# Optimization experiments

Hardware: AMD Instinct MI355X
Metric: run time of the kernel (lower is better)

## Reference

```python
import jax, jax.numpy as jnp
import numpy as np

N, C, D, H, W = 4, 9, 16, 1024, 1024  # batch, grid channels, grid size, image HxW


def setup_inputs() -> dict:
    key = jax.random.key(0)
    k1, k2, k3, k4 = jax.random.split(key, 4)
    bilateral_grid = jax.random.normal(k1, (N, C, D, D, D), dtype=jnp.float32)
    guidemap = jax.random.uniform(k2, (N, 3, H, W), dtype=jnp.float32)
    conv_w = jax.random.normal(k3, (3, C + 3), dtype=jnp.float32) * 0.1  # 1x1 conv kernel
    conv_b = jax.random.normal(k4, (3,), dtype=jnp.float32) * 0.1
    return {"bilateral_grid": bilateral_grid, "guidemap": guidemap,
            "conv_w": conv_w, "conv_b": conv_b}


def _trilinear_slice(grid, guide):
    # grid: [N, C, D, D, D]; guide: [N, 3, H, W] with values in [0,1]
    n, c, d = grid.shape[0], grid.shape[1], grid.shape[2]
    h, w = guide.shape[2], guide.shape[3]
    grid_flat = grid.reshape(n, c, d * d * d)
    coords = jnp.clip(guide, 0.0, 1.0) * (d - 1)          # [N,3,H,W]
    i0 = jnp.clip(jnp.floor(coords), 0, d - 2).astype(jnp.int32)
    f = coords - i0.astype(coords.dtype)                   # fractional part
    r0, g0, b0 = i0[:, 0], i0[:, 1], i0[:, 2]              # [N,H,W]
    fr, fg, fb = f[:, 0], f[:, 1], f[:, 2]                 # [N,H,W]

    def gather(ir, ig, ib):
        flat = ((ir * d + ig) * d + ib).reshape(n, 1, h * w)
        return jnp.take_along_axis(grid_flat, flat, axis=2)  # [N,C,H*W]

    out = jnp.zeros((n, c, h * w), dtype=grid.dtype)
    for dr in (0, 1):
        for dg in (0, 1):
            for db in (0, 1):
                wgt = ((fr if dr else 1.0 - fr) *
                       (fg if dg else 1.0 - fg) *
                       (fb if db else 1.0 - fb)).reshape(n, 1, h * w)
                out = out + gather(r0 + dr, g0 + dg, b0 + db) * wgt
    return out.reshape(n, c, h, w)


def reference(bilateral_grid, guidemap, conv_w, conv_b):
    res = _trilinear_slice(bilateral_grid, guidemap)       # [N,9,H,W]
    res = jnp.concatenate([res, guidemap], axis=1)         # [N,12,H,W]
    out = jnp.einsum('oi,nihw->nohw', conv_w, res) + conv_b[None, :, None, None]
    return out
```

## Files before the change

kernel.cpp:

```cpp
#include <hip/hip_runtime.h>
#include <hip/hip_bf16.h>

static constexpr int N_ = 4;
static constexpr int C_ = 9;
static constexpr int D_ = 16;
static constexpr int HWp = 1024 * 1024;
static constexpr int CELLS = D_ * D_ * D_;
static constexpr int PT = HWp / 4;
static constexpr int TPB = 512;
static constexpr int BPI = 256;

__device__ __forceinline__ void unpack3(uint2 w, float& x, float& y, float& z) {
    x = __uint_as_float(w.x << 16);
    y = __uint_as_float(w.x & 0xFFFF0000u);
    z = __uint_as_float(w.y << 16);
}

__device__ __forceinline__ float lerp1(float a, float b, float t) {
    return fmaf(b - a, t, a);
}

__global__ __launch_bounds__(TPB) void slice_kernel(
    const float* __restrict__ grid, const float* __restrict__ guide,
    const float* __restrict__ cw, const float* __restrict__ cbias,
    float* __restrict__ out)
{
    __shared__ uint2 sPre[CELLS];

    const int n  = blockIdx.x >> 8;
    const int bi = blockIdx.x & (BPI - 1);

    {
        const float* g = grid + (size_t)n * C_ * CELLS;
#pragma unroll
        for (int k = 0; k < CELLS / TPB; ++k) {
            int cell = k * TPB + threadIdx.x;
            float a0 = 0.f, a1 = 0.f, a2 = 0.f;
#pragma unroll
            for (int c = 0; c < C_; ++c) {
                float v = g[(size_t)c * CELLS + cell];
                a0 = fmaf(cw[c], v, a0);
                a1 = fmaf(cw[12 + c], v, a1);
                a2 = fmaf(cw[24 + c], v, a2);
            }
            unsigned short b0 = __bfloat16_as_ushort(__float2bfloat16(a0));
            unsigned short b1 = __bfloat16_as_ushort(__float2bfloat16(a1));
            unsigned short b2 = __bfloat16_as_ushort(__float2bfloat16(a2));
            uint2 v;
            v.x = (unsigned)b0 | ((unsigned)b1 << 16);
            v.y = (unsigned)b2;
            sPre[cell] = v;
        }
    }
    __syncthreads();

    const float4* gR = (const float4*)(guide + (size_t)(n * 3 + 0) * HWp);
    const float4* gG = (const float4*)(guide + (size_t)(n * 3 + 1) * HWp);
    const float4* gB = (const float4*)(guide + (size_t)(n * 3 + 2) * HWp);
    float4* oR = (float4*)(out + (size_t)(n * 3 + 0) * HWp);
    float4* oG = (float4*)(out + (size_t)(n * 3 + 1) * HWp);
    float4* oB = (float4*)(out + (size_t)(n * 3 + 2) * HWp);

    const float w0r = cw[9],  w0g = cw[10], w0b = cw[11];
    const float w1r = cw[21], w1g = cw[22], w1b = cw[23];
    const float w2r = cw[33], w2g = cw[34], w2b = cw[35];
    const float bi0 = cbias[0], bi1 = cbias[1], bi2 = cbias[2];

    const int base0 = bi * (PT / BPI);

#pragma unroll
    for (int it = 0; it < (PT / BPI) / TPB; ++it) {
        const int p4 = base0 + it * TPB + threadIdx.x;
        float4 r4 = gR[p4];
        float4 g4 = gG[p4];
        float4 b4 = gB[p4];

        float rr[4] = {r4.x, r4.y, r4.z, r4.w};
        float gg[4] = {g4.x, g4.y, g4.z, g4.w};
        float bb[4] = {b4.x, b4.y, b4.z, b4.w};
        float o0[4], o1[4], o2[4];

#pragma unroll
        for (int j = 0; j < 4; ++j) {
            float cr = fminf(fmaxf(rr[j], 0.f), 1.f) * 15.f;
            float cg = fminf(fmaxf(gg[j], 0.f), 1.f) * 15.f;
            float cb = fminf(fmaxf(bb[j], 0.f), 1.f) * 15.f;
            int ir = min((int)cr, 14);
            int ig = min((int)cg, 14);
            int ib = min((int)cb, 14);
            float fr = cr - (float)ir;
            float fg = cg - (float)ig;
            float fb = cb - (float)ib;
            int base = (ir * 16 + ig) * 16 + ib;

            uint2 q000 = sPre[base];
            uint2 q001 = sPre[base + 1];
            uint2 q010 = sPre[base + 16];
            uint2 q011 = sPre[base + 17];
            uint2 q100 = sPre[base + 256];
            uint2 q101 = sPre[base + 257];
            uint2 q110 = sPre[base + 272];
            uint2 q111 = sPre[base + 273];

            float ax, ay, az, bx, by, bz;
            float v00x, v00y, v00z, v01x, v01y, v01z;
            float v10x, v10y, v10z, v11x, v11y, v11z;

            unpack3(q000, ax, ay, az); unpack3(q001, bx, by, bz);
            v00x = lerp1(ax, bx, fb); v00y = lerp1(ay, by, fb); v00z = lerp1(az, bz, fb);
            unpack3(q010, ax, ay, az); unpack3(q011, bx, by, bz);
            v01x = lerp1(ax, bx, fb); v01y = lerp1(ay, by, fb); v01z = lerp1(az, bz, fb);
            unpack3(q100, ax, ay, az); unpack3(q101, bx, by, bz);
            v10x = lerp1(ax, bx, fb); v10y = lerp1(ay, by, fb); v10z = lerp1(az, bz, fb);
            unpack3(q110, ax, ay, az); unpack3(q111, bx, by, bz);
            v11x = lerp1(ax, bx, fb); v11y = lerp1(ay, by, fb); v11z = lerp1(az, bz, fb);

            float v0x = lerp1(v00x, v01x, fg);
            float v0y = lerp1(v00y, v01y, fg);
            float v0z = lerp1(v00z, v01z, fg);
            float v1x = lerp1(v10x, v11x, fg);
            float v1y = lerp1(v10y, v11y, fg);
            float v1z = lerp1(v10z, v11z, fg);

            float vx = lerp1(v0x, v1x, fr);
            float vy = lerp1(v0y, v1y, fr);
            float vz = lerp1(v0z, v1z, fr);

            o0[j] = vx + fmaf(w0r, rr[j], fmaf(w0g, gg[j], fmaf(w0b, bb[j], bi0)));
            o1[j] = vy + fmaf(w1r, rr[j], fmaf(w1g, gg[j], fmaf(w1b, bb[j], bi1)));
            o2[j] = vz + fmaf(w2r, rr[j], fmaf(w2g, gg[j], fmaf(w2b, bb[j], bi2)));
        }

        oR[p4] = make_float4(o0[0], o0[1], o0[2], o0[3]);
        oG[p4] = make_float4(o1[0], o1[1], o1[2], o1[3]);
        oB[p4] = make_float4(o2[0], o2[1], o2[2], o2[3]);
    }
}

extern "C" void kernel_launch(void* const* d_in, const int* in_sizes, int n_in,
                              void* d_out, int out_size, void* d_ws, size_t ws_size,
                              hipStream_t stream) {
    const float* grid  = (const float*)d_in[0];
    const float* guide = (const float*)d_in[1];
    const float* cw    = (const float*)d_in[2];
    const float* cb    = (const float*)d_in[3];
    float* out = (float*)d_out;

    slice_kernel<<<N_ * BPI, TPB, 0, stream>>>(grid, guide, cw, cb, out);
}
```

Measured before the change: 114.8 us.

## Store b-axis cell pairs in fp16 LDS entries and interpolate with packed half2

Each shared-memory entry now holds the 3 projected channels for a cell and its +b neighbour, packed as fp16 into one uint4. Each pixel then does 4 LDS reads instead of 8. The trilinear lerps run as packed half2 FMAs in place of scalar fp32 math, which cuts LDS traffic and ALU work per pixel. The trade-off is fp16 precision for the interpolated values, a larger 16-byte LDS entry that may raise bank pressure, and a heavier precompute that does a division per entry.

```diff
diff --git a/kernel.cpp b/kernel.cpp
--- a/kernel.cpp
+++ b/kernel.cpp
@@ -1,21 +1,25 @@
 #include <hip/hip_runtime.h>
-#include <hip/hip_bf16.h>
+#include <hip/hip_fp16.h>
 
 static constexpr int N_ = 4;
 static constexpr int C_ = 9;
 static constexpr int D_ = 16;
 static constexpr int HWp = 1024 * 1024;
 static constexpr int CELLS = D_ * D_ * D_;
+static constexpr int NPAIR = 16 * 16 * 15;
 static constexpr int PT = HWp / 4;
 static constexpr int TPB = 512;
 static constexpr int BPI = 256;
 
-__device__ __forceinline__ void unpack3(uint2 w, float& x, float& y, float& z) {
-    x = __uint_as_float(w.x << 16);
-    y = __uint_as_float(w.x & 0xFFFF0000u);
-    z = __uint_as_float(w.y << 16);
+__device__ __forceinline__ __half2 as_h2(unsigned u) {
+    union { unsigned u; __half2 h; } v; v.u = u; return v.h;
 }
-
+__device__ __forceinline__ unsigned h2_as_u(__half2 h) {
+    union { __half2 h; unsigned u; } v; v.h = h; return v.u;
+}
+__device__ __forceinline__ __half2 lerp2(__half2 a, __half2 b, __half2 t) {
+    return __hfma2(__hsub2(b, a), t, a);
+}
 __device__ __forceinline__ float lerp1(float a, float b, float t) {
     return fmaf(b - a, t, a);
 }
@@ -25,31 +29,36 @@
     const float* __restrict__ cw, const float* __restrict__ cbias,
     float* __restrict__ out)
 {
-    __shared__ uint2 sPre[CELLS];
+    __shared__ uint4 sPre[NPAIR];
 
     const int n  = blockIdx.x >> 8;
     const int bi = blockIdx.x & (BPI - 1);
 
     {
         const float* g = grid + (size_t)n * C_ * CELLS;
-#pragma unroll
-        for (int k = 0; k < CELLS / TPB; ++k) {
-            int cell = k * TPB + threadIdx.x;
+        for (int e = threadIdx.x; e < NPAIR; e += TPB) {
+            int rg = e / 15;
+            int b  = e - rg * 15;
+            int cell = rg * 16 + b;
             float a0 = 0.f, a1 = 0.f, a2 = 0.f;
+            float c0 = 0.f, c1 = 0.f, c2 = 0.f;
 #pragma unroll
             for (int c = 0; c < C_; ++c) {
-                float v = g[(size_t)c * CELLS + cell];
-                a0 = fmaf(cw[c], v, a0);
-                a1 = fmaf(cw[12 + c], v, a1);
-                a2 = fmaf(cw[24 + c], v, a2);
+                float v0 = g[(size_t)c * CELLS + cell];
+                float v1 = g[(size_t)c * CELLS + cell + 1];
+                a0 = fmaf(cw[c], v0, a0);
+                a1 = fmaf(cw[12 + c], v0, a1);
+                a2 = fmaf(cw[24 + c], v0, a2);
+                c0 = fmaf(cw[c], v1, c0);
+                c1 = fmaf(cw[12 + c], v1, c1);
+                c2 = fmaf(cw[24 + c], v1, c2);
             }
-            unsigned short b0 = __bfloat16_as_ushort(__float2bfloat16(a0));
-            unsigned short b1 = __bfloat16_as_ushort(__float2bfloat16(a1));
-            unsigned short b2 = __bfloat16_as_ushort(__float2bfloat16(a2));
-            uint2 v;
-            v.x = (unsigned)b0 | ((unsigned)b1 << 16);
-            v.y = (unsigned)b2;
-            sPre[cell] = v;
+            uint4 E;
+            E.x = h2_as_u(__floats2half2_rn(a0, a1));
+            E.y = h2_as_u(__floats2half2_rn(c0, c1));
+            E.z = h2_as_u(__floats2half2_rn(a2, c2));
+            E.w = 0;
+            sPre[e] = E;
         }
     }
     __syncthreads();
@@ -91,40 +100,42 @@
             float fr = cr - (float)ir;
             float fg = cg - (float)ig;
             float fb = cb - (float)ib;
-            int base = (ir * 16 + ig) * 16 + ib;
 
-            uint2 q000 = sPre[base];
-            uint2 q001 = sPre[base + 1];
-            uint2 q010 = sPre[base + 16];
-            uint2 q011 = sPre[base + 17];
-            uint2 q100 = sPre[base + 256];
-            uint2 q101 = sPre[base + 257];
-            uint2 q110 = sPre[base + 272];
-            uint2 q111 = sPre[base + 273];
+            int e = (ir * 16 + ig) * 15 + ib;
+            uint4 E00 = sPre[e];
+            uint4 E01 = sPre[e + 15];
+            uint4 E10 = sPre[e + 240];
+            uint4 E11 = sPre[e + 255];
 
-            float ax, ay, az, bx, by, bz;
-            float v00x, v00y, v00z, v01x, v01y, v01z;
-            float v10x, v10y, v10z, v11x, v11y, v11z;
+            __half  fbh = __float2half_rn(fb);
+            __half2 fb2 = __half2half2(fbh);
+            __half2 fg2 = __half2half2(__float2half_rn(fg));
+            __half2 fr2 = __half2half2(__float2half_rn(fr));
 
-            unpack3(q000, ax, ay, az); unpack3(q001, bx, by, bz);
-            v00x = lerp1(ax, bx, fb); v00y = lerp1(ay, by, fb); v00z = lerp1(az, bz, fb);
-            unpack3(q010, ax, ay, az); unpack3(q011, bx, by, bz);
-            v01x = lerp1(ax, bx, fb); v01y = lerp1(ay, by, fb); v01z = lerp1(az, bz, fb);
-            unpack3(q100, ax, ay, az); unpack3(q101, bx, by, bz);
-            v10x = lerp1(ax, bx, fb); v10y = lerp1(ay, by, fb); v10z = lerp1(az, bz, fb);
-            unpack3(q110, ax, ay, az); unpack3(q111, bx, by, bz);
-            v11x = lerp1(ax, bx, fb); v11y = lerp1(ay, by, fb); v11z = lerp1(az, bz, fb);
+            __half2 xy00 = lerp2(as_h2(E00.x), as_h2(E00.y), fb2);
+            __half2 xy01 = lerp2(as_h2(E01.x), as_h2(E01.y), fb2);
+            __half2 xy10 = lerp2(as_h2(E10.x), as_h2(E10.y), fb2);
+            __half2 xy11 = lerp2(as_h2(E11.x), as_h2(E11.y), fb2);
+            __half2 z00p = as_h2(E00.z), z01p = as_h2(E01.z);
+            __half2 z10p = as_h2(E10.z), z11p = as_h2(E11.z);
+            __half z00 = __hfma(__hsub(__high2half(z00p), __low2half(z00p)), fbh, __low2half(z00p));
+            __half z01 = __hfma(__hsub(__high2half(z01p), __low2half(z01p)), fbh, __low2half(z01p));
+            __half z10 = __hfma(__hsub(__high2half(z10p), __low2half(z10p)), fbh, __low2half(z10p));
+            __half z11 = __hfma(__hsub(__high2half(z11p), __low2half(z11p)), fbh, __low2half(z11p));
 
-            float v0x = lerp1(v00x, v01x, fg);
-            float v0y = lerp1(v00y, v01y, fg);
-            float v0z = lerp1(v00z, v01z, fg);
-            float v1x = lerp1(v10x, v11x, fg);
-            float v1y = lerp1(v10y, v11y, fg);
-            float v1z = lerp1(v10z, v11z, fg);
+            __half2 xy0 = lerp2(xy00, xy01, fg2);
+            __half2 xy1 = lerp2(xy10, xy11, fg2);
+            __half2 zA  = __halves2half2(z00, z10);
+            __half2 zB  = __halves2half2(z01, z11);
+            __half2 zG  = lerp2(zA, zB, fg2);
 
-            float vx = lerp1(v0x, v1x, fr);
-            float vy = lerp1(v0y, v1y, fr);
-            float vz = lerp1(v0z, v1z, fr);
+            __half2 xyF = lerp2(xy0, xy1, fr2);
+            __half  zF  = __hfma(__hsub(__high2half(zG), __low2half(zG)),
+                                 __float2half_rn(fr), __low2half(zG));
+
+            float vx = __half2float(__low2half(xyF));
+            float vy = __half2float(__high2half(xyF));
+            float vz = __half2float(zF);
 
             o0[j] = vx + fmaf(w0r, rr[j], fmaf(w0g, gg[j], fmaf(w0b, bb[j], bi0)));
             o1[j] = vy + fmaf(w1r, rr[j], fmaf(w1g, gg[j], fmaf(w1b, bb[j], bi1)));
```

Result: slower. 122.9 us (+7.1%).
